# Optimization experiments

Measured on AMD Instinct MI355X. Metric: run time of the kernel, lower is better.

## Reference

```python
import jax, jax.numpy as jnp
import numpy as np

TOPK = 2
ROUTE_SCALE = 1.0


def setup_inputs() -> dict:
    key = jax.random.key(0)
    ks = jax.random.split(key, 9)
    B, T, C, E, H = 4, 2048, 1024, 8, 2752
    s = 0.02  # init scale for weights
    return {
        "x": jax.random.normal(ks[0], (B, T, C), dtype=jnp.float32),
        "gate_w": jax.random.normal(ks[1], (E, C), dtype=jnp.float32) * s,
        "expert_bias": jnp.zeros((E,), dtype=jnp.float32),
        "w1": jax.random.normal(ks[2], (E, C, H), dtype=jnp.float32) * s,
        "w2": jax.random.normal(ks[3], (E, H, C), dtype=jnp.float32) * s,
        "w3": jax.random.normal(ks[4], (E, C, H), dtype=jnp.float32) * s,
        "sw1": jax.random.normal(ks[5], (C, H), dtype=jnp.float32) * s,
        "sw2": jax.random.normal(ks[6], (H, C), dtype=jnp.float32) * s,
        "sw3": jax.random.normal(ks[7], (C, H), dtype=jnp.float32) * s,
    }


def reference(x, gate_w, expert_bias, w1, w2, w3, sw1, sw2, sw3):
    B, T, C = x.shape
    E = gate_w.shape[0]
    xf = x.reshape(-1, C)  # (N, C)
    N = xf.shape[0]

    # --- ExpertGate (sigmoid scoring, aux-loss-free, eval mode) ---
    scores = jax.nn.sigmoid(xf @ gate_w.T)            # (N, E), original scores
    routing = scores + expert_bias[None, :]           # bias only affects selection
    _, idx = jax.lax.top_k(routing, TOPK)             # (N, TOPK)
    w = jnp.take_along_axis(scores, idx, axis=1)      # gather original scores
    w = w / (w.sum(axis=-1, keepdims=True) + 1e-8)    # sigmoid normalization
    w = w * ROUTE_SCALE

    # Scatter top-k weights into a dense (N, E) combine matrix
    gates = jnp.zeros((N, E), dtype=xf.dtype)
    gates = gates.at[jnp.arange(N)[:, None], idx].add(w)

    # --- Routed SwiGLU experts (dense compute, gated combine) ---
    y = jnp.zeros_like(xf)
    for e in range(E):  # small fixed loop over experts
        h = jax.nn.silu(xf @ w1[e]) * (xf @ w3[e])    # (N, H)
        y = y + gates[:, e:e + 1] * (h @ w2[e])

    # --- Shared expert (always on) ---
    y = y + (jax.nn.silu(xf @ sw1) * (xf @ sw3)) @ sw2

    return y.reshape(B, T, C)
```

## Files before the change

### kernel.cpp

```cpp
#include <hip/hip_runtime.h>
#include <hip/hip_bf16.h>
#include <stdint.h>

#define E_ 8
#define C_ 1024
#define H_ 2752
#define NTOK 8192
#define CAP_ROWS 17408

typedef unsigned short u16;
typedef __attribute__((ext_vector_type(8))) short bf16x8;
typedef __attribute__((ext_vector_type(4))) float f32x4;

static constexpr size_t SZ_XB    = (size_t)NTOK * C_ * 2;
static constexpr size_t SZ_WT    = (size_t)E_ * H_ * C_ * 2;
static constexpr size_t SZ_SWT   = (size_t)H_ * C_ * 2;
static constexpr size_t SZ_H     = (size_t)CAP_ROWS * H_ * 2;

static constexpr size_t OFF_XB   = 0;
static constexpr size_t OFF_W1T  = OFF_XB   + SZ_XB;
static constexpr size_t OFF_W3T  = OFF_W1T  + SZ_WT;
static constexpr size_t OFF_W2T  = OFF_W3T  + SZ_WT;
static constexpr size_t OFF_SW1T = OFF_W2T  + SZ_WT;
static constexpr size_t OFF_SW3T = OFF_SW1T + SZ_SWT;
static constexpr size_t OFF_SW2T = OFF_SW3T + SZ_SWT;
static constexpr size_t OFF_H    = OFF_SW2T + SZ_SWT;
static constexpr size_t OFF_RIDX = OFF_H    + SZ_H;
static constexpr size_t OFF_RW   = OFF_RIDX + (size_t)NTOK*2*4;
static constexpr size_t OFF_OFFS = OFF_RW   + (size_t)NTOK*2*4;
static constexpr size_t OFF_PTOK = OFF_OFFS + 64;
static constexpr size_t OFF_PW   = OFF_PTOK + (size_t)CAP_ROWS*4;
static constexpr size_t WS_NEED  = OFF_PW   + (size_t)CAP_ROWS*4;

__device__ __forceinline__ u16 f2bf(float f) {
  union { float f; uint32_t u; } v; v.f = f;
  uint32_t r = v.u + 0x7FFFu + ((v.u >> 16) & 1u);
  return (u16)(r >> 16);
}

__device__ __forceinline__ void gld16(const void* g, const void* l) {
  uint32_t lo = (uint32_t)(uintptr_t)l;
  lo = __builtin_amdgcn_readfirstlane(lo);
  __builtin_amdgcn_global_load_lds(
      (const __attribute__((address_space(1))) void*)g,
      (__attribute__((address_space(3))) void*)(uintptr_t)lo, 16, 0, 0);
}

#define MFMA16(A,B,C) __builtin_amdgcn_mfma_f32_16x16x32_bf16((A),(B),(C),0,0,0)

__global__ __launch_bounds__(256) void gate_kernel(
    const float* __restrict__ x, const float* __restrict__ gw,
    const float* __restrict__ bias, u16* __restrict__ xb,
    int* __restrict__ ridx, float* __restrict__ rw)
{
  const int n = blockIdx.x, t = threadIdx.x;
  const float4 v = *(const float4*)(x + (size_t)n * C_ + t * 4);
  union { u16 u[4]; uint2 d; } pk;
  pk.u[0] = f2bf(v.x); pk.u[1] = f2bf(v.y); pk.u[2] = f2bf(v.z); pk.u[3] = f2bf(v.w);
  *(uint2*)(xb + (size_t)n * C_ + t * 4) = pk.d;

  float p[E_];
#pragma unroll
  for (int e = 0; e < E_; ++e) {
    const float4 g = *(const float4*)(gw + (size_t)e * C_ + t * 4);
    p[e] = v.x * g.x + v.y * g.y + v.z * g.z + v.w * g.w;
  }
#pragma unroll
  for (int e = 0; e < E_; ++e)
    for (int off = 32; off > 0; off >>= 1) p[e] += __shfl_down(p[e], off);

  __shared__ float red[4][E_];
  const int wv = t >> 6;
  if ((t & 63) == 0) {
#pragma unroll
    for (int e = 0; e < E_; ++e) red[wv][e] = p[e];
  }
  __syncthreads();
  if (t == 0) {
    float sc[E_], rt[E_];
#pragma unroll
    for (int e = 0; e < E_; ++e) {
      const float d = red[0][e] + red[1][e] + red[2][e] + red[3][e];
      const float s = 1.f / (1.f + expf(-d));
      sc[e] = s; rt[e] = s + bias[e];
    }
    int i0 = 0; float b0 = rt[0];
#pragma unroll
    for (int e = 1; e < E_; ++e) if (rt[e] > b0) { b0 = rt[e]; i0 = e; }
    int i1 = -1; float b1 = -1e30f;
#pragma unroll
    for (int e = 0; e < E_; ++e) if (e != i0 && rt[e] > b1) { b1 = rt[e]; i1 = e; }
    const float s0 = sc[i0], s1 = sc[i1];
    const float inv = 1.f / (s0 + s1 + 1e-8f);
    ridx[2 * n] = i0; ridx[2 * n + 1] = i1;
    rw[2 * n] = s0 * inv; rw[2 * n + 1] = s1 * inv;
  }
}

__global__ __launch_bounds__(256) void transpose_cs_kernel(
    const float* __restrict__ w1, const float* __restrict__ w3,
    const float* __restrict__ sw1, const float* __restrict__ sw3,
    u16* __restrict__ w1t, u16* __restrict__ w3t,
    u16* __restrict__ sw1t, u16* __restrict__ sw3t)
{
  const int z = blockIdx.z;
  const float* src; u16* dst;
  if      (z < 8)  { src = w1 + (size_t)z * C_ * H_;       dst = w1t + (size_t)z * H_ * C_; }
  else if (z < 16) { src = w3 + (size_t)(z - 8) * C_ * H_; dst = w3t + (size_t)(z - 8) * H_ * C_; }
  else if (z == 16){ src = sw1; dst = sw1t; }
  else             { src = sw3; dst = sw3t; }
  __shared__ float tile[32][33];
  const int tx = threadIdx.x, ty = threadIdx.y;
  const int s0 = blockIdx.x * 32;
  const int r0 = blockIdx.y * 32;
#pragma unroll
  for (int i = 0; i < 4; ++i)
    tile[ty + 8 * i][tx] = src[(size_t)(r0 + ty + 8 * i) * H_ + s0 + tx];
  __syncthreads();
#pragma unroll
  for (int i = 0; i < 4; ++i)
    dst[(size_t)(s0 + ty + 8 * i) * C_ + r0 + tx] = f2bf(tile[tx][ty + 8 * i]);
}

__global__ __launch_bounds__(256) void transpose_sc_kernel(
    const float* __restrict__ w2, const float* __restrict__ sw2,
    u16* __restrict__ w2t, u16* __restrict__ sw2t)
{
  const int z = blockIdx.z;
  const float* src; u16* dst;
  if (z < 8) { src = w2 + (size_t)z * H_ * C_; dst = w2t + (size_t)z * C_ * H_; }
  else       { src = sw2; dst = sw2t; }
  __shared__ float tile[32][33];
  const int tx = threadIdx.x, ty = threadIdx.y;
  const int s0 = blockIdx.x * 32;
  const int r0 = blockIdx.y * 32;
#pragma unroll
  for (int i = 0; i < 4; ++i)
    tile[ty + 8 * i][tx] = src[(size_t)(r0 + ty + 8 * i) * C_ + s0 + tx];
  __syncthreads();
#pragma unroll
  for (int i = 0; i < 4; ++i)
    dst[(size_t)(s0 + ty + 8 * i) * H_ + r0 + tx] = f2bf(tile[tx][ty + 8 * i]);
}

__global__ __launch_bounds__(256) void route_scan_kernel(
    const int* __restrict__ ridx, const float* __restrict__ rw,
    int* __restrict__ offsets, int* __restrict__ perm_tok, float* __restrict__ perm_w)
{
  __shared__ int cnt[256][E_];
  __shared__ int pref[E_][257];
  __shared__ int offs[E_ + 1];
  __shared__ int totals[E_];
  const int t = threadIdx.x;
#pragma unroll
  for (int e = 0; e < E_; ++e) cnt[t][e] = 0;
  for (int j = 0; j < 64; ++j) { const int e = ridx[t * 64 + j]; cnt[t][e]++; }
  __syncthreads();
  if (t < E_) {
    int run = 0;
    for (int i = 0; i < 256; ++i) { pref[t][i] = run; run += cnt[i][t]; }
    totals[t] = run; pref[t][256] = run;
  }
  __syncthreads();
  if (t == 0) {
    int o = 0;
    for (int e = 0; e < E_; ++e) { offs[e] = o; o += (totals[e] + 127) & ~127; }
    offs[E_] = o;
    for (int i = 0; i <= E_; ++i) offsets[i] = offs[i];
  }
  __syncthreads();
#pragma unroll
  for (int e = 0; e < E_; ++e) cnt[t][e] = offs[e] + pref[e][t];
  for (int j = 0; j < 64; ++j) {
    const int a = t * 64 + j;
    const int e = ridx[a];
    const int p = cnt[t][e]++;
    perm_tok[p] = a >> 1;
    perm_w[p] = rw[a];
  }
  __syncthreads();
  for (int e = 0; e < E_; ++e) {
    for (int p = offs[e] + totals[e] + t; p < offs[e + 1]; p += 256) {
      perm_tok[p] = 0; perm_w[p] = 0.f;
    }
  }
}

template<int GATHER>
__global__ __launch_bounds__(256, 2) void gemm1_kernel(
    const u16* __restrict__ xb, const u16* __restrict__ w1t_all,
    const u16* __restrict__ w3t_all, u16* __restrict__ hout,
    const int* __restrict__ offsets, const int* __restrict__ perm_tok)
{
  __shared__ u16 lds[3 * 8192];
  const int t = threadIdx.x;
  const int row0 = blockIdx.x * 128;
  const int n0 = blockIdx.y * 128;
  int e = 0;
  if (GATHER) {
    if (row0 >= offsets[8]) return;
#pragma unroll
    for (int i = 0; i < 7; ++i) if (row0 >= offsets[i + 1]) e = i + 1;
  }
  const u16* w1t = GATHER ? (w1t_all + (size_t)e * (H_ * C_)) : w1t_all;
  const u16* w3t = GATHER ? (w3t_all + (size_t)e * (H_ * C_)) : w3t_all;

  const int tq = t >> 3;
  const int cb = (((t & 7) ^ (tq & 7)) << 4);
  const char* gA[4]; const char* gB1[4]; const char* gB3[4];
#pragma unroll
  for (int i = 0; i < 4; ++i) {
    const int m = i * 32 + tq;
    const int tok = GATHER ? perm_tok[row0 + m] : (row0 + m);
    gA[i]  = (const char*)xb  + (size_t)tok * (C_ * 2) + cb;
    const int nn = n0 + m;
    gB1[i] = (const char*)w1t + (size_t)nn * (C_ * 2) + cb;
    gB3[i] = (const char*)w3t + (size_t)nn * (C_ * 2) + cb;
  }
  char* lwave = (char*)lds + (t >> 6) * 1024;

  f32x4 acc1[4][4], acc3[4][4];
#pragma unroll
  for (int i = 0; i < 4; ++i)
#pragma unroll
    for (int j = 0; j < 4; ++j) { acc1[i][j] = f32x4{0.f,0.f,0.f,0.f}; acc3[i][j] = f32x4{0.f,0.f,0.f,0.f}; }

  const int lane = t & 63;
  const int l15 = lane & 15, lhi = lane >> 4, swz = lane & 7;
  const int wm = (t >> 7) & 1, wn = (t >> 6) & 1;
  int arow[4], brow[4];
#pragma unroll
  for (int f = 0; f < 4; ++f) {
    arow[f] = (wm * 64 + f * 16 + l15) * 128;
    brow[f] = (wn * 64 + f * 16 + l15) * 128;
  }
  const char* ldsc = (const char*)lds;

  for (int kt = 0; kt < C_ / 64; ++kt) {
    const int kb = kt * 128;
#pragma unroll
    for (int i = 0; i < 4; ++i) gld16(gA[i]  + kb, lwave + i * 4096);
#pragma unroll
    for (int i = 0; i < 4; ++i) gld16(gB1[i] + kb, lwave + 16384 + i * 4096);
#pragma unroll
    for (int i = 0; i < 4; ++i) gld16(gB3[i] + kb, lwave + 32768 + i * 4096);
    __syncthreads();
#pragma unroll
    for (int kk = 0; kk < 2; ++kk) {
      const int co = ((((kk << 2) | lhi)) ^ swz) << 4;
      bf16x8 a[4], b1[4], b3[4];
#pragma unroll
      for (int f = 0; f < 4; ++f) a[f]  = *(const bf16x8*)(ldsc + arow[f] + co);
#pragma unroll
      for (int f = 0; f < 4; ++f) b1[f] = *(const bf16x8*)(ldsc + 16384 + brow[f] + co);
#pragma unroll
      for (int f = 0; f < 4; ++f) b3[f] = *(const bf16x8*)(ldsc + 32768 + brow[f] + co);
#pragma unroll
      for (int mf = 0; mf < 4; ++mf)
#pragma unroll
        for (int nf = 0; nf < 4; ++nf) {
          acc1[mf][nf] = MFMA16(a[mf], b1[nf], acc1[mf][nf]);
          acc3[mf][nf] = MFMA16(a[mf], b3[nf], acc3[mf][nf]);
        }
    }
    __syncthreads();
  }

  const int rbase = row0 + wm * 64 + lhi * 4;
  const int cbase = n0 + wn * 64 + l15;
#pragma unroll
  for (int mf = 0; mf < 4; ++mf)
#pragma unroll
    for (int q = 0; q < 4; ++q) {
      const int r = rbase + mf * 16 + q;
      u16* hrow = hout + (size_t)r * H_;
#pragma unroll
      for (int nf = 0; nf < 4; ++nf) {
        const int c = cbase + nf * 16;
        if (c < H_) {
          const float v1 = acc1[mf][nf][q], v3 = acc3[mf][nf][q];
          const float sv = v1 / (1.f + __expf(-v1));
          hrow[c] = f2bf(sv * v3);
        }
      }
    }
}

template<int MODE>
__global__ __launch_bounds__(256, 2) void gemm2_kernel(
    const u16* __restrict__ hin, const u16* __restrict__ w2t_all,
    float* __restrict__ y, const int* __restrict__ offsets,
    const int* __restrict__ perm_tok, const float* __restrict__ perm_w)
{
  __shared__ u16 lds[2 * 8192];
  const int t = threadIdx.x;
  const int row0 = blockIdx.x * 128;
  const int n0 = blockIdx.y * 128;
  int e = 0;
  if (MODE == 1) {
    if (row0 >= offsets[8]) return;
#pragma unroll
    for (int i = 0; i < 7; ++i) if (row0 >= offsets[i + 1]) e = i + 1;
  }
  const u16* w2t = (MODE == 1) ? (w2t_all + (size_t)e * (C_ * H_)) : w2t_all;

  const int tq = t >> 3;
  const int cb = (((t & 7) ^ (tq & 7)) << 4);
  const char* gA[4]; const char* gB[4];
#pragma unroll
  for (int i = 0; i < 4; ++i) {
    gA[i] = (const char*)hin + (size_t)(row0 + i * 32 + tq) * (H_ * 2) + cb;
    gB[i] = (const char*)w2t + (size_t)(n0  + i * 32 + tq) * (H_ * 2) + cb;
  }
  char* lwave = (char*)lds + (t >> 6) * 1024;

  f32x4 acc[4][4];
#pragma unroll
  for (int i = 0; i < 4; ++i)
#pragma unroll
    for (int j = 0; j < 4; ++j) acc[i][j] = f32x4{0.f,0.f,0.f,0.f};

  const int lane = t & 63;
  const int l15 = lane & 15, lhi = lane >> 4, swz = lane & 7;
  const int wm = (t >> 7) & 1, wn = (t >> 6) & 1;
  int arow[4], brow[4];
#pragma unroll
  for (int f = 0; f < 4; ++f) {
    arow[f] = (wm * 64 + f * 16 + l15) * 128;
    brow[f] = (wn * 64 + f * 16 + l15) * 128;
  }
  const char* ldsc = (const char*)lds;

  for (int kt = 0; kt < H_ / 64; ++kt) {
    const int kb = kt * 128;
#pragma unroll
    for (int i = 0; i < 4; ++i) gld16(gA[i] + kb, lwave + i * 4096);
#pragma unroll
    for (int i = 0; i < 4; ++i) gld16(gB[i] + kb, lwave + 16384 + i * 4096);
    __syncthreads();
#pragma unroll
    for (int kk = 0; kk < 2; ++kk) {
      const int co = ((((kk << 2) | lhi)) ^ swz) << 4;
      bf16x8 a[4], b[4];
#pragma unroll
      for (int f = 0; f < 4; ++f) a[f] = *(const bf16x8*)(ldsc + arow[f] + co);
#pragma unroll
      for (int f = 0; f < 4; ++f) b[f] = *(const bf16x8*)(ldsc + 16384 + brow[f] + co);
#pragma unroll
      for (int mf = 0; mf < 4; ++mf)
#pragma unroll
        for (int nf = 0; nf < 4; ++nf)
          acc[mf][nf] = MFMA16(a[mf], b[nf], acc[mf][nf]);
    }
    __syncthreads();
  }

  const int rbase = row0 + wm * 64 + lhi * 4;
  const int cbase = n0 + wn * 64 + l15;
#pragma unroll
  for (int mf = 0; mf < 4; ++mf)
#pragma unroll
    for (int q = 0; q < 4; ++q) {
      const int r = rbase + mf * 16 + q;
      if (MODE == 0) {
        float* yr = y + (size_t)r * C_;
#pragma unroll
        for (int nf = 0; nf < 4; ++nf) yr[cbase + nf * 16] = acc[mf][nf][q];
      } else {
        const float wgt = perm_w[r];
        if (wgt != 0.f) {
          const int tok = perm_tok[r];
          float* yr = y + (size_t)tok * C_;
#pragma unroll
          for (int nf = 0; nf < 4; ++nf)
            atomicAdd(yr + cbase + nf * 16, wgt * acc[mf][nf][q]);
        }
      }
    }
}

extern "C" void kernel_launch(void* const* d_in, const int* in_sizes, int n_in,
                              void* d_out, int out_size, void* d_ws, size_t ws_size,
                              hipStream_t stream)
{
  const float* x    = (const float*)d_in[0];
  const float* gw   = (const float*)d_in[1];
  const float* bias = (const float*)d_in[2];
  const float* w1   = (const float*)d_in[3];
  const float* w2   = (const float*)d_in[4];
  const float* w3   = (const float*)d_in[5];
  const float* sw1  = (const float*)d_in[6];
  const float* sw2  = (const float*)d_in[7];
  const float* sw3  = (const float*)d_in[8];
  float* y = (float*)d_out;
  char* ws = (char*)d_ws;
  if (ws_size < WS_NEED) return;

  u16*   xb    = (u16*)(ws + OFF_XB);
  u16*   w1t   = (u16*)(ws + OFF_W1T);
  u16*   w3t   = (u16*)(ws + OFF_W3T);
  u16*   w2t   = (u16*)(ws + OFF_W2T);
  u16*   sw1t  = (u16*)(ws + OFF_SW1T);
  u16*   sw3t  = (u16*)(ws + OFF_SW3T);
  u16*   sw2t  = (u16*)(ws + OFF_SW2T);
  u16*   hbuf  = (u16*)(ws + OFF_H);
  int*   ridx  = (int*)(ws + OFF_RIDX);
  float* rwt   = (float*)(ws + OFF_RW);
  int*   offs  = (int*)(ws + OFF_OFFS);
  int*   ptok  = (int*)(ws + OFF_PTOK);
  float* pw    = (float*)(ws + OFF_PW);

  gate_kernel<<<NTOK, 256, 0, stream>>>(x, gw, bias, xb, ridx, rwt);
  transpose_cs_kernel<<<dim3(H_ / 32, C_ / 32, 18), dim3(32, 8), 0, stream>>>(
      w1, w3, sw1, sw3, w1t, w3t, sw1t, sw3t);
  transpose_sc_kernel<<<dim3(C_ / 32, H_ / 32, 9), dim3(32, 8), 0, stream>>>(
      w2, sw2, w2t, sw2t);
  route_scan_kernel<<<1, 256, 0, stream>>>(ridx, rwt, offs, ptok, pw);

  gemm1_kernel<0><<<dim3(NTOK / 128, 22), 256, 0, stream>>>(
      xb, sw1t, sw3t, hbuf, nullptr, nullptr);
  gemm2_kernel<0><<<dim3(NTOK / 128, 8), 256, 0, stream>>>(
      hbuf, sw2t, y, nullptr, nullptr, nullptr);
  gemm1_kernel<1><<<dim3(CAP_ROWS / 128, 22), 256, 0, stream>>>(
      xb, w1t, w3t, hbuf, offs, ptok);
  gemm2_kernel<1><<<dim3(CAP_ROWS / 128, 8), 256, 0, stream>>>(
      hbuf, w2t, y, offs, ptok, pw);
}
```

Baseline: 671.9 us.

## Rewrite expert GEMMs as 256x128 tiles with 8-wave pipelined LDS prefetch

Replaces the 128x128 tile GEMMs with 512-thread, 256x128-tile kernels that double-buffer K-slices in LDS. Global-to-LDS loads are issued ahead of the MFMA work using explicit vmcnt waits, raw barriers and setprio. The shared-expert and routed-expert first GEMMs are merged into a single launch, and routing capacity is padded to 256-row blocks. The K tail of the second GEMM reads from a zeroed pad buffer instead of branching. This aims to hide memory latency and raise MFMA utilisation, at the cost of more padded rows, a much larger LDS footprint, and fragile hand-tuned synchronisation.

Result: slower. 786.8 us (+17.1%).

```diff
diff --git a/kernel.cpp b/kernel.cpp
--- a/kernel.cpp
+++ b/kernel.cpp
@@ -6,7 +6,11 @@
 #define C_ 1024
 #define H_ 2752
 #define NTOK 8192
-#define CAP_ROWS 17408
+#define CAP_ROWS 18432
+#define ROUTED_MB 72
+#define SHARED_MB 32
+#define SHARED_HBASE 18432
+#define HROWS 26624
 
 typedef unsigned short u16;
 typedef __attribute__((ext_vector_type(8))) short bf16x8;
@@ -15,7 +19,7 @@
 static constexpr size_t SZ_XB    = (size_t)NTOK * C_ * 2;
 static constexpr size_t SZ_WT    = (size_t)E_ * H_ * C_ * 2;
 static constexpr size_t SZ_SWT   = (size_t)H_ * C_ * 2;
-static constexpr size_t SZ_H     = (size_t)CAP_ROWS * H_ * 2;
+static constexpr size_t SZ_H     = (size_t)HROWS * H_ * 2;
 
 static constexpr size_t OFF_XB   = 0;
 static constexpr size_t OFF_W1T  = OFF_XB   + SZ_XB;
@@ -25,7 +29,8 @@
 static constexpr size_t OFF_SW3T = OFF_SW1T + SZ_SWT;
 static constexpr size_t OFF_SW2T = OFF_SW3T + SZ_SWT;
 static constexpr size_t OFF_H    = OFF_SW2T + SZ_SWT;
-static constexpr size_t OFF_RIDX = OFF_H    + SZ_H;
+static constexpr size_t OFF_ZP   = OFF_H    + SZ_H;
+static constexpr size_t OFF_RIDX = OFF_ZP   + 16384;
 static constexpr size_t OFF_RW   = OFF_RIDX + (size_t)NTOK*2*4;
 static constexpr size_t OFF_OFFS = OFF_RW   + (size_t)NTOK*2*4;
 static constexpr size_t OFF_PTOK = OFF_OFFS + 64;
@@ -38,7 +43,7 @@
   return (u16)(r >> 16);
 }
 
-__device__ __forceinline__ void gld16(const void* g, const void* l) {
+__device__ __forceinline__ void gld16(const void* g, void* l) {
   uint32_t lo = (uint32_t)(uintptr_t)l;
   lo = __builtin_amdgcn_readfirstlane(lo);
   __builtin_amdgcn_global_load_lds(
@@ -47,6 +52,9 @@
 }
 
 #define MFMA16(A,B,C) __builtin_amdgcn_mfma_f32_16x16x32_bf16((A),(B),(C),0,0,0)
+#define BARX() do { asm volatile("" ::: "memory"); __builtin_amdgcn_s_barrier(); \
+                    asm volatile("" ::: "memory"); } while (0)
+#define VMC(N) asm volatile("s_waitcnt vmcnt(" #N ")" ::: "memory")
 
 __global__ __launch_bounds__(256) void gate_kernel(
     const float* __restrict__ x, const float* __restrict__ gw,
@@ -164,7 +172,7 @@
   __syncthreads();
   if (t == 0) {
     int o = 0;
-    for (int e = 0; e < E_; ++e) { offs[e] = o; o += (totals[e] + 127) & ~127; }
+    for (int e = 0; e < E_; ++e) { offs[e] = o; o += (totals[e] + 255) & ~255; }
     offs[E_] = o;
     for (int i = 0; i <= E_; ++i) offsets[i] = offs[i];
   }
@@ -186,197 +194,251 @@
   }
 }
 
-template<int GATHER>
-__global__ __launch_bounds__(256, 2) void gemm1_kernel(
+__global__ __launch_bounds__(512, 2) void gemm1_8p(
     const u16* __restrict__ xb, const u16* __restrict__ w1t_all,
-    const u16* __restrict__ w3t_all, u16* __restrict__ hout,
-    const int* __restrict__ offsets, const int* __restrict__ perm_tok)
-{
-  __shared__ u16 lds[3 * 8192];
+    const u16* __restrict__ w3t_all, const u16* __restrict__ sw1t,
+    const u16* __restrict__ sw3t, u16* __restrict__ hbuf,
+    const int* __restrict__ offsets, const int* __restrict__ ptok)
+{
+  __shared__ char lds[131072];
   const int t = threadIdx.x;
-  const int row0 = blockIdx.x * 128;
+  const int bx = blockIdx.x;
   const int n0 = blockIdx.y * 128;
-  int e = 0;
-  if (GATHER) {
+
+  const u16 *b1w, *b3w; int row0; size_t hr0; int gather;
+  if (bx < ROUTED_MB) {
+    row0 = bx * 256;
     if (row0 >= offsets[8]) return;
+    int e = 0;
 #pragma unroll
     for (int i = 0; i < 7; ++i) if (row0 >= offsets[i + 1]) e = i + 1;
-  }
-  const u16* w1t = GATHER ? (w1t_all + (size_t)e * (H_ * C_)) : w1t_all;
-  const u16* w3t = GATHER ? (w3t_all + (size_t)e * (H_ * C_)) : w3t_all;
-
-  const int tq = t >> 3;
-  const int cb = (((t & 7) ^ (tq & 7)) << 4);
-  const char* gA[4]; const char* gB1[4]; const char* gB3[4];
-#pragma unroll
-  for (int i = 0; i < 4; ++i) {
-    const int m = i * 32 + tq;
-    const int tok = GATHER ? perm_tok[row0 + m] : (row0 + m);
-    gA[i]  = (const char*)xb  + (size_t)tok * (C_ * 2) + cb;
-    const int nn = n0 + m;
-    gB1[i] = (const char*)w1t + (size_t)nn * (C_ * 2) + cb;
-    gB3[i] = (const char*)w3t + (size_t)nn * (C_ * 2) + cb;
-  }
-  char* lwave = (char*)lds + (t >> 6) * 1024;
-
-  f32x4 acc1[4][4], acc3[4][4];
-#pragma unroll
-  for (int i = 0; i < 4; ++i)
-#pragma unroll
-    for (int j = 0; j < 4; ++j) { acc1[i][j] = f32x4{0.f,0.f,0.f,0.f}; acc3[i][j] = f32x4{0.f,0.f,0.f,0.f}; }
-
-  const int lane = t & 63;
-  const int l15 = lane & 15, lhi = lane >> 4, swz = lane & 7;
-  const int wm = (t >> 7) & 1, wn = (t >> 6) & 1;
-  int arow[4], brow[4];
-#pragma unroll
-  for (int f = 0; f < 4; ++f) {
-    arow[f] = (wm * 64 + f * 16 + l15) * 128;
-    brow[f] = (wn * 64 + f * 16 + l15) * 128;
-  }
-  const char* ldsc = (const char*)lds;
-
-  for (int kt = 0; kt < C_ / 64; ++kt) {
-    const int kb = kt * 128;
-#pragma unroll
-    for (int i = 0; i < 4; ++i) gld16(gA[i]  + kb, lwave + i * 4096);
-#pragma unroll
-    for (int i = 0; i < 4; ++i) gld16(gB1[i] + kb, lwave + 16384 + i * 4096);
-#pragma unroll
-    for (int i = 0; i < 4; ++i) gld16(gB3[i] + kb, lwave + 32768 + i * 4096);
-    __syncthreads();
-#pragma unroll
-    for (int kk = 0; kk < 2; ++kk) {
-      const int co = ((((kk << 2) | lhi)) ^ swz) << 4;
-      bf16x8 a[4], b1[4], b3[4];
-#pragma unroll
-      for (int f = 0; f < 4; ++f) a[f]  = *(const bf16x8*)(ldsc + arow[f] + co);
-#pragma unroll
-      for (int f = 0; f < 4; ++f) b1[f] = *(const bf16x8*)(ldsc + 16384 + brow[f] + co);
-#pragma unroll
-      for (int f = 0; f < 4; ++f) b3[f] = *(const bf16x8*)(ldsc + 32768 + brow[f] + co);
-#pragma unroll
-      for (int mf = 0; mf < 4; ++mf)
-#pragma unroll
-        for (int nf = 0; nf < 4; ++nf) {
-          acc1[mf][nf] = MFMA16(a[mf], b1[nf], acc1[mf][nf]);
-          acc3[mf][nf] = MFMA16(a[mf], b3[nf], acc3[mf][nf]);
-        }
-    }
-    __syncthreads();
-  }
-
-  const int rbase = row0 + wm * 64 + lhi * 4;
-  const int cbase = n0 + wn * 64 + l15;
-#pragma unroll
-  for (int mf = 0; mf < 4; ++mf)
+    b1w = w1t_all + (size_t)e * (H_ * C_);
+    b3w = w3t_all + (size_t)e * (H_ * C_);
+    hr0 = (size_t)row0; gather = 1;
+  } else {
+    row0 = (bx - ROUTED_MB) * 256;
+    b1w = sw1t; b3w = sw3t; hr0 = (size_t)SHARED_HBASE + row0; gather = 0;
+  }
+
+  const int sr = t >> 2, sc = (t & 3) << 4;
+  const int ta0 = gather ? ptok[row0 + sr]       : (row0 + sr);
+  const int ta1 = gather ? ptok[row0 + 128 + sr] : (row0 + 128 + sr);
+  const char* aS0 = (const char*)xb + (size_t)ta0 * 2048 + sc;
+  const char* aS1 = (const char*)xb + (size_t)ta1 * 2048 + sc;
+  int nb = n0 + sr; if (nb > H_ - 1) nb = H_ - 1;
+  const char* b1S = (const char*)b1w + (size_t)nb * 2048 + sc;
+  const char* b3S = (const char*)b3w + (size_t)nb * 2048 + sc;
+  const int wb = (t >> 6) << 10;
+  char* ldsp = (char*)lds;
+
+#define ARG(kt,kh)  ((((kt)&1)*2+(kh))*16384)
+#define B1RG(kt,kh) (65536 + ((((kt)&1)*2+(kh))*8192))
+#define B3RG(kt,kh) (98304 + ((((kt)&1)*2+(kh))*8192))
+#define SA(kt,kh) do { const int go=(kt)*128+(kh)*64; \
+  gld16(aS0+go, ldsp+ARG(kt,kh)+wb); gld16(aS1+go, ldsp+ARG(kt,kh)+8192+wb); } while(0)
+#define SB(kt,kh) do { const int go=(kt)*128+(kh)*64; \
+  gld16(b1S+go, ldsp+B1RG(kt,kh)+wb); gld16(b3S+go, ldsp+B3RG(kt,kh)+wb); } while(0)
+
+  const int lane = t & 63, l15 = lane & 15, lhi = lane >> 4;
+  const int wv = t >> 6, wm = wv >> 2, wn = wv & 3;
+  int aoff[8], boff[2];
+#pragma unroll
+  for (int mf = 0; mf < 8; ++mf) aoff[mf] = (wm * 128 + mf * 16 + l15) * 64 + lhi * 16;
+#pragma unroll
+  for (int nf = 0; nf < 2; ++nf) boff[nf] = (wn * 32 + nf * 16 + l15) * 64 + lhi * 16;
+
+  bf16x8 a[4], rb1[2], rb3[2];
+  f32x4 acc1[8][2], acc3[8][2];
+#pragma unroll
+  for (int i = 0; i < 8; ++i)
+#pragma unroll
+    for (int j = 0; j < 2; ++j) { acc1[i][j] = f32x4{0,0,0,0}; acc3[i][j] = f32x4{0,0,0,0}; }
+
+#define LB(kt,kh) do { \
+  rb1[0]=*(const bf16x8*)(ldsp+B1RG(kt,kh)+boff[0]); \
+  rb1[1]=*(const bf16x8*)(ldsp+B1RG(kt,kh)+boff[1]); \
+  rb3[0]=*(const bf16x8*)(ldsp+B3RG(kt,kh)+boff[0]); \
+  rb3[1]=*(const bf16x8*)(ldsp+B3RG(kt,kh)+boff[1]); } while(0)
+#define LA(kt,kh,mh) do { \
+  a[0]=*(const bf16x8*)(ldsp+ARG(kt,kh)+aoff[(mh)*4+0]); \
+  a[1]=*(const bf16x8*)(ldsp+ARG(kt,kh)+aoff[(mh)*4+1]); \
+  a[2]=*(const bf16x8*)(ldsp+ARG(kt,kh)+aoff[(mh)*4+2]); \
+  a[3]=*(const bf16x8*)(ldsp+ARG(kt,kh)+aoff[(mh)*4+3]); } while(0)
+#define MM(mh) do { __builtin_amdgcn_s_setprio(1); \
+  _Pragma("unroll") for (int mf = 0; mf < 4; ++mf) \
+    _Pragma("unroll") for (int nf = 0; nf < 2; ++nf) { \
+      acc1[(mh)*4+mf][nf] = MFMA16(a[mf], rb1[nf], acc1[(mh)*4+mf][nf]); \
+      acc3[(mh)*4+mf][nf] = MFMA16(a[mf], rb3[nf], acc3[(mh)*4+mf][nf]); } \
+  __builtin_amdgcn_s_setprio(0); } while(0)
+
+  SA(0,0); SA(0,1); SB(0,0); SB(0,1); SA(1,0); SB(1,0);
+  VMC(4); BARX();
+
+#pragma unroll 1
+  for (int i = 0; i < 8; ++i) {
+    const int k0 = 2*i, k1 = k0+1, k2 = k0+2, k3 = k0+3;
+    const bool more = (i < 7);
+    LB(k0,0); LA(k0,0,0); SA(k1,1); SB(k1,1);
+    BARX(); MM(0); BARX();
+    LA(k0,0,1);
+    BARX(); MM(1); BARX();
+    LB(k0,1); LA(k0,1,0); if (more) SA(k2,0);
+    BARX(); MM(0); BARX();
+    LA(k0,1,1); if (more) SB(k2,0);
+    BARX(); MM(1); VMC(4); BARX();
+    LB(k1,0); LA(k1,0,0); if (more) { SA(k2,1); SB(k2,1); }
+    BARX(); MM(0); BARX();
+    LA(k1,0,1);
+    BARX(); MM(1); BARX();
+    LB(k1,1); LA(k1,1,0); if (more) SA(k3,0);
+    BARX(); MM(0); BARX();
+    LA(k1,1,1); if (more) SB(k3,0);
+    BARX(); MM(1); VMC(4); BARX();
+  }
+
+  const int rb_ = wm * 128 + lhi * 4;
+  const int cb_ = n0 + wn * 32 + l15;
+#pragma unroll
+  for (int mf = 0; mf < 8; ++mf)
 #pragma unroll
     for (int q = 0; q < 4; ++q) {
-      const int r = rbase + mf * 16 + q;
-      u16* hrow = hout + (size_t)r * H_;
-#pragma unroll
-      for (int nf = 0; nf < 4; ++nf) {
-        const int c = cbase + nf * 16;
+      const int r = rb_ + mf * 16 + q;
+      u16* hrow = hbuf + (hr0 + r) * H_;
+#pragma unroll
+      for (int nf = 0; nf < 2; ++nf) {
+        const int c = cb_ + nf * 16;
         if (c < H_) {
           const float v1 = acc1[mf][nf][q], v3 = acc3[mf][nf][q];
-          const float sv = v1 / (1.f + __expf(-v1));
-          hrow[c] = f2bf(sv * v3);
+          hrow[c] = f2bf((v1 / (1.f + __expf(-v1))) * v3);
         }
       }
     }
+#undef ARG
+#undef B1RG
+#undef B3RG
+#undef SA
+#undef SB
+#undef LB
+#undef LA
+#undef MM
 }
 
 template<int MODE>
-__global__ __launch_bounds__(256, 2) void gemm2_kernel(
-    const u16* __restrict__ hin, const u16* __restrict__ w2t_all,
+__global__ __launch_bounds__(512, 2) void gemm2_8p(
+    const u16* __restrict__ hbuf, const u16* __restrict__ w2t_all,
     float* __restrict__ y, const int* __restrict__ offsets,
-    const int* __restrict__ perm_tok, const float* __restrict__ perm_w)
-{
-  __shared__ u16 lds[2 * 8192];
+    const int* __restrict__ ptok, const float* __restrict__ pw,
+    const char* __restrict__ zp)
+{
+  __shared__ char lds[98304];
   const int t = threadIdx.x;
-  const int row0 = blockIdx.x * 128;
+  const int bx = blockIdx.x;
   const int n0 = blockIdx.y * 128;
-  int e = 0;
+
+  int row0 = bx * 256; size_t hr0; const u16* bW;
   if (MODE == 1) {
     if (row0 >= offsets[8]) return;
+    int e = 0;
 #pragma unroll
     for (int i = 0; i < 7; ++i) if (row0 >= offsets[i + 1]) e = i + 1;
-  }
-  const u16* w2t = (MODE == 1) ? (w2t_all + (size_t)e * (C_ * H_)) : w2t_all;
-
-  const int tq = t >> 3;
-  const int cb = (((t & 7) ^ (tq & 7)) << 4);
-  const char* gA[4]; const char* gB[4];
-#pragma unroll
-  for (int i = 0; i < 4; ++i) {
-    gA[i] = (const char*)hin + (size_t)(row0 + i * 32 + tq) * (H_ * 2) + cb;
-    gB[i] = (const char*)w2t + (size_t)(n0  + i * 32 + tq) * (H_ * 2) + cb;
-  }
-  char* lwave = (char*)lds + (t >> 6) * 1024;
-
-  f32x4 acc[4][4];
-#pragma unroll
-  for (int i = 0; i < 4; ++i)
-#pragma unroll
-    for (int j = 0; j < 4; ++j) acc[i][j] = f32x4{0.f,0.f,0.f,0.f};
-
-  const int lane = t & 63;
-  const int l15 = lane & 15, lhi = lane >> 4, swz = lane & 7;
-  const int wm = (t >> 7) & 1, wn = (t >> 6) & 1;
-  int arow[4], brow[4];
-#pragma unroll
-  for (int f = 0; f < 4; ++f) {
-    arow[f] = (wm * 64 + f * 16 + l15) * 128;
-    brow[f] = (wn * 64 + f * 16 + l15) * 128;
-  }
-  const char* ldsc = (const char*)lds;
-
-  for (int kt = 0; kt < H_ / 64; ++kt) {
-    const int kb = kt * 128;
-#pragma unroll
-    for (int i = 0; i < 4; ++i) gld16(gA[i] + kb, lwave + i * 4096);
-#pragma unroll
-    for (int i = 0; i < 4; ++i) gld16(gB[i] + kb, lwave + 16384 + i * 4096);
-    __syncthreads();
-#pragma unroll
-    for (int kk = 0; kk < 2; ++kk) {
-      const int co = ((((kk << 2) | lhi)) ^ swz) << 4;
-      bf16x8 a[4], b[4];
-#pragma unroll
-      for (int f = 0; f < 4; ++f) a[f] = *(const bf16x8*)(ldsc + arow[f] + co);
-#pragma unroll
-      for (int f = 0; f < 4; ++f) b[f] = *(const bf16x8*)(ldsc + 16384 + brow[f] + co);
-#pragma unroll
-      for (int mf = 0; mf < 4; ++mf)
-#pragma unroll
-        for (int nf = 0; nf < 4; ++nf)
-          acc[mf][nf] = MFMA16(a[mf], b[nf], acc[mf][nf]);
-    }
-    __syncthreads();
-  }
-
-  const int rbase = row0 + wm * 64 + lhi * 4;
-  const int cbase = n0 + wn * 64 + l15;
-#pragma unroll
-  for (int mf = 0; mf < 4; ++mf)
+    bW = w2t_all + (size_t)e * (C_ * H_);
+    hr0 = (size_t)row0;
+  } else {
+    bW = w2t_all;
+    hr0 = (size_t)SHARED_HBASE + row0;
+  }
+
+  const int sr = t >> 2, sc = (t & 3) << 4;
+  const char* aS0 = (const char*)hbuf + (hr0 + sr) * (size_t)(H_ * 2) + sc;
+  const char* aS1 = (const char*)hbuf + (hr0 + 128 + sr) * (size_t)(H_ * 2) + sc;
+  const char* bS  = (const char*)bW + (size_t)(n0 + sr) * (H_ * 2) + sc;
+  const int wb = (t >> 6) << 10;
+  char* ldsp = (char*)lds;
+  const char* zpa = zp + t * 16;
+  const char* zpb = zp + t * 16;
+
+#define A2RG(kt,kh) ((((kt)&1)*2+(kh))*16384)
+#define B2RG(kt,kh) (65536 + ((((kt)&1)*2+(kh))*8192))
+#define SA2(kt,kh) do { if ((kt) < 43) { const int go=(kt)*128+(kh)*64; \
+    gld16(aS0+go, ldsp+A2RG(kt,kh)+wb); gld16(aS1+go, ldsp+A2RG(kt,kh)+8192+wb); } \
+  else { gld16(zpa, ldsp+A2RG(kt,kh)+wb); gld16(zpa, ldsp+A2RG(kt,kh)+8192+wb); } } while(0)
+#define SB2(kt,kh) do { if ((kt) < 43) { const int go=(kt)*128+(kh)*64; \
+    gld16(bS+go, ldsp+B2RG(kt,kh)+wb); } \
+  else { gld16(zpb, ldsp+B2RG(kt,kh)+wb); } } while(0)
+
+  const int lane = t & 63, l15 = lane & 15, lhi = lane >> 4;
+  const int wv = t >> 6, wm = wv >> 2, wn = wv & 3;
+  int aoff[8], boff[2];
+#pragma unroll
+  for (int mf = 0; mf < 8; ++mf) aoff[mf] = (wm * 128 + mf * 16 + l15) * 64 + lhi * 16;
+#pragma unroll
+  for (int nf = 0; nf < 2; ++nf) boff[nf] = (wn * 32 + nf * 16 + l15) * 64 + lhi * 16;
+
+  bf16x8 a8[8], rb[2];
+  f32x4 acc[8][2];
+#pragma unroll
+  for (int i = 0; i < 8; ++i)
+#pragma unroll
+    for (int j = 0; j < 2; ++j) acc[i][j] = f32x4{0,0,0,0};
+
+#define LB2(kt,kh) do { \
+  rb[0]=*(const bf16x8*)(ldsp+B2RG(kt,kh)+boff[0]); \
+  rb[1]=*(const bf16x8*)(ldsp+B2RG(kt,kh)+boff[1]); } while(0)
+#define LA8(kt,kh) do { \
+  _Pragma("unroll") for (int mf = 0; mf < 8; ++mf) \
+    a8[mf]=*(const bf16x8*)(ldsp+A2RG(kt,kh)+aoff[mf]); } while(0)
+#define MM2() do { __builtin_amdgcn_s_setprio(1); \
+  _Pragma("unroll") for (int mf = 0; mf < 8; ++mf) \
+    _Pragma("unroll") for (int nf = 0; nf < 2; ++nf) \
+      acc[mf][nf] = MFMA16(a8[mf], rb[nf], acc[mf][nf]); \
+  __builtin_amdgcn_s_setprio(0); } while(0)
+
+  SA2(0,0); SA2(0,1); SB2(0,0); SB2(0,1); SA2(1,0); SB2(1,0);
+  VMC(3); BARX();
+
+#pragma unroll 1
+  for (int i = 0; i < 22; ++i) {
+    const int k0 = 2*i, k1 = k0+1, k2 = k0+2, k3 = k0+3;
+    const bool more = (i < 21);
+    LB2(k0,0); LA8(k0,0); SA2(k1,1); SB2(k1,1);
+    BARX(); MM2(); BARX();
+    LB2(k0,1); LA8(k0,1); if (more) { SA2(k2,0); SB2(k2,0); }
+    BARX(); MM2(); VMC(3); BARX();
+    LB2(k1,0); LA8(k1,0); if (more) { SA2(k2,1); SB2(k2,1); }
+    BARX(); MM2(); BARX();
+    LB2(k1,1); LA8(k1,1); if (more) { SA2(k3,0); SB2(k3,0); }
+    BARX(); MM2(); VMC(3); BARX();
+  }
+
+  const int rb_ = wm * 128 + lhi * 4;
+  const int cb_ = n0 + wn * 32 + l15;
+#pragma unroll
+  for (int mf = 0; mf < 8; ++mf)
 #pragma unroll
     for (int q = 0; q < 4; ++q) {
-      const int r = rbase + mf * 16 + q;
+      const int r = rb_ + mf * 16 + q;
       if (MODE == 0) {
-        float* yr = y + (size_t)r * C_;
-#pragma unroll
-        for (int nf = 0; nf < 4; ++nf) yr[cbase + nf * 16] = acc[mf][nf][q];
+        float* yr = y + (size_t)(row0 + r) * C_;
+#pragma unroll
+        for (int nf = 0; nf < 2; ++nf) yr[cb_ + nf * 16] = acc[mf][nf][q];
       } else {
-        const float wgt = perm_w[r];
+        const float wgt = pw[row0 + r];
         if (wgt != 0.f) {
-          const int tok = perm_tok[r];
+          const int tok = ptok[row0 + r];
           float* yr = y + (size_t)tok * C_;
 #pragma unroll
-          for (int nf = 0; nf < 4; ++nf)
-            atomicAdd(yr + cbase + nf * 16, wgt * acc[mf][nf][q]);
+          for (int nf = 0; nf < 2; ++nf)
+            atomicAdd(yr + cb_ + nf * 16, wgt * acc[mf][nf][q]);
         }
       }
     }
+#undef A2RG
+#undef B2RG
+#undef SA2
+#undef SB2
+#undef LB2
+#undef LA8
+#undef MM2
 }
 
 extern "C" void kernel_launch(void* const* d_in, const int* in_sizes, int n_in,
@@ -404,12 +466,14 @@
   u16*   sw3t  = (u16*)(ws + OFF_SW3T);
   u16*   sw2t  = (u16*)(ws + OFF_SW2T);
   u16*   hbuf  = (u16*)(ws + OFF_H);
+  char*  zp    = ws + OFF_ZP;
   int*   ridx  = (int*)(ws + OFF_RIDX);
   float* rwt   = (float*)(ws + OFF_RW);
   int*   offs  = (int*)(ws + OFF_OFFS);
   int*   ptok  = (int*)(ws + OFF_PTOK);
   float* pw    = (float*)(ws + OFF_PW);
 
+  hipMemsetAsync(zp, 0, 16384, stream);
   gate_kernel<<<NTOK, 256, 0, stream>>>(x, gw, bias, xb, ridx, rwt);
   transpose_cs_kernel<<<dim3(H_ / 32, C_ / 32, 18), dim3(32, 8), 0, stream>>>(
       w1, w3, sw1, sw3, w1t, w3t, sw1t, sw3t);
@@ -417,12 +481,10 @@
       w2, sw2, w2t, sw2t);
   route_scan_kernel<<<1, 256, 0, stream>>>(ridx, rwt, offs, ptok, pw);
 
-  gemm1_kernel<0><<<dim3(NTOK / 128, 22), 256, 0, stream>>>(
-      xb, sw1t, sw3t, hbuf, nullptr, nullptr);
-  gemm2_kernel<0><<<dim3(NTOK / 128, 8), 256, 0, stream>>>(
-      hbuf, sw2t, y, nullptr, nullptr, nullptr);
-  gemm1_kernel<1><<<dim3(CAP_ROWS / 128, 22), 256, 0, stream>>>(
-      xb, w1t, w3t, hbuf, offs, ptok);
-  gemm2_kernel<1><<<dim3(CAP_ROWS / 128, 8), 256, 0, stream>>>(
-      hbuf, w2t, y, offs, ptok, pw);
-}
+  gemm1_8p<<<dim3(ROUTED_MB + SHARED_MB, 22), 512, 0, stream>>>(
+      xb, w1t, w3t, sw1t, sw3t, hbuf, offs, ptok);
+  gemm2_8p<0><<<dim3(SHARED_MB, 8), 512, 0, stream>>>(
+      hbuf, sw2t, y, offs, ptok, pw, zp);
+  gemm2_8p<1><<<dim3(ROUTED_MB, 8), 512, 0, stream>>>(
+      hbuf, w2t, y, offs, ptok, pw, zp);
+}
```

## Switch GEMMs to 32x32 MFMA and merge shared and routed experts into single launches

Applied to the files above, without the earlier changes.

Both GEMM kernels move from 16x16x32 to 32x32x16 bf16 MFMA tiles, with fewer, larger accumulator fragments per wave. The shared-expert and routed-expert GEMMs are fused into one launch each by extending the grid, so shared rows use a separate region of the enlarged H buffer. The shared output is now accumulated with atomics, which requires a memset of y first. The aim is higher MFMA throughput per LDS read and fewer launches and tail effects, at the cost of extra atomics for the shared path and a larger workspace.

New measurement: 732.2 us. 9.0% more time.

```diff
diff --git a/kernel.cpp b/kernel.cpp
--- a/kernel.cpp
+++ b/kernel.cpp
@@ -7,15 +7,19 @@
 #define H_ 2752
 #define NTOK 8192
 #define CAP_ROWS 17408
+#define ROUTED_XB1 136
+#define SHARED_XB1 64
+#define SHARED_HBASE 17408
+#define HROWS 25600
 
 typedef unsigned short u16;
 typedef __attribute__((ext_vector_type(8))) short bf16x8;
-typedef __attribute__((ext_vector_type(4))) float f32x4;
+typedef __attribute__((ext_vector_type(16))) float f32x16;
 
 static constexpr size_t SZ_XB    = (size_t)NTOK * C_ * 2;
 static constexpr size_t SZ_WT    = (size_t)E_ * H_ * C_ * 2;
 static constexpr size_t SZ_SWT   = (size_t)H_ * C_ * 2;
-static constexpr size_t SZ_H     = (size_t)CAP_ROWS * H_ * 2;
+static constexpr size_t SZ_H     = (size_t)HROWS * H_ * 2;
 
 static constexpr size_t OFF_XB   = 0;
 static constexpr size_t OFF_W1T  = OFF_XB   + SZ_XB;
@@ -38,7 +42,7 @@
   return (u16)(r >> 16);
 }
 
-__device__ __forceinline__ void gld16(const void* g, const void* l) {
+__device__ __forceinline__ void gld16(const void* g, void* l) {
   uint32_t lo = (uint32_t)(uintptr_t)l;
   lo = __builtin_amdgcn_readfirstlane(lo);
   __builtin_amdgcn_global_load_lds(
@@ -46,7 +50,7 @@
       (__attribute__((address_space(3))) void*)(uintptr_t)lo, 16, 0, 0);
 }
 
-#define MFMA16(A,B,C) __builtin_amdgcn_mfma_f32_16x16x32_bf16((A),(B),(C),0,0,0)
+#define MFMA32(A,B,C) __builtin_amdgcn_mfma_f32_32x32x16_bf16((A),(B),(C),0,0,0)
 
 __global__ __launch_bounds__(256) void gate_kernel(
     const float* __restrict__ x, const float* __restrict__ gw,
@@ -186,24 +190,31 @@
   }
 }
 
-template<int GATHER>
-__global__ __launch_bounds__(256, 2) void gemm1_kernel(
+__global__ __launch_bounds__(256, 2) void gemm1_32(
     const u16* __restrict__ xb, const u16* __restrict__ w1t_all,
-    const u16* __restrict__ w3t_all, u16* __restrict__ hout,
-    const int* __restrict__ offsets, const int* __restrict__ perm_tok)
-{
-  __shared__ u16 lds[3 * 8192];
+    const u16* __restrict__ w3t_all, const u16* __restrict__ sw1t,
+    const u16* __restrict__ sw3t, u16* __restrict__ hbuf,
+    const int* __restrict__ offsets, const int* __restrict__ ptok)
+{
+  __shared__ char lds[49152];
   const int t = threadIdx.x;
-  const int row0 = blockIdx.x * 128;
+  const int bx = blockIdx.x;
   const int n0 = blockIdx.y * 128;
-  int e = 0;
-  if (GATHER) {
+
+  const u16 *b1w, *b3w; int row0; size_t hr0; int gather;
+  if (bx < ROUTED_XB1) {
+    row0 = bx * 128;
     if (row0 >= offsets[8]) return;
+    int e = 0;
 #pragma unroll
     for (int i = 0; i < 7; ++i) if (row0 >= offsets[i + 1]) e = i + 1;
-  }
-  const u16* w1t = GATHER ? (w1t_all + (size_t)e * (H_ * C_)) : w1t_all;
-  const u16* w3t = GATHER ? (w3t_all + (size_t)e * (H_ * C_)) : w3t_all;
+    b1w = w1t_all + (size_t)e * (H_ * C_);
+    b3w = w3t_all + (size_t)e * (H_ * C_);
+    hr0 = (size_t)row0; gather = 1;
+  } else {
+    row0 = (bx - ROUTED_XB1) * 128;
+    b1w = sw1t; b3w = sw3t; hr0 = (size_t)SHARED_HBASE + row0; gather = 0;
+  }
 
   const int tq = t >> 3;
   const int cb = (((t & 7) ^ (tq & 7)) << 4);
@@ -211,170 +222,171 @@
 #pragma unroll
   for (int i = 0; i < 4; ++i) {
     const int m = i * 32 + tq;
-    const int tok = GATHER ? perm_tok[row0 + m] : (row0 + m);
-    gA[i]  = (const char*)xb  + (size_t)tok * (C_ * 2) + cb;
-    const int nn = n0 + m;
-    gB1[i] = (const char*)w1t + (size_t)nn * (C_ * 2) + cb;
-    gB3[i] = (const char*)w3t + (size_t)nn * (C_ * 2) + cb;
-  }
-  char* lwave = (char*)lds + (t >> 6) * 1024;
-
-  f32x4 acc1[4][4], acc3[4][4];
-#pragma unroll
-  for (int i = 0; i < 4; ++i)
-#pragma unroll
-    for (int j = 0; j < 4; ++j) { acc1[i][j] = f32x4{0.f,0.f,0.f,0.f}; acc3[i][j] = f32x4{0.f,0.f,0.f,0.f}; }
-
-  const int lane = t & 63;
-  const int l15 = lane & 15, lhi = lane >> 4, swz = lane & 7;
+    const int tok = gather ? ptok[row0 + m] : (row0 + m);
+    gA[i] = (const char*)xb + (size_t)tok * 2048 + cb;
+    int nn = n0 + m; if (nn > H_ - 1) nn = H_ - 1;
+    gB1[i] = (const char*)b1w + (size_t)nn * 2048 + cb;
+    gB3[i] = (const char*)b3w + (size_t)nn * 2048 + cb;
+  }
+  const int wvb = (t >> 6) << 10;
+  char* ldsp = (char*)lds;
+
+  const int lane = t & 63, l31 = lane & 31, hi = lane >> 5, x7 = lane & 7;
   const int wm = (t >> 7) & 1, wn = (t >> 6) & 1;
-  int arow[4], brow[4];
-#pragma unroll
-  for (int f = 0; f < 4; ++f) {
-    arow[f] = (wm * 64 + f * 16 + l15) * 128;
-    brow[f] = (wn * 64 + f * 16 + l15) * 128;
-  }
-  const char* ldsc = (const char*)lds;
-
-  for (int kt = 0; kt < C_ / 64; ++kt) {
+  int arow[2], brow[2];
+#pragma unroll
+  for (int f = 0; f < 2; ++f) {
+    arow[f] = (wm * 64 + f * 32 + l31) * 128;
+    brow[f] = (wn * 64 + f * 32 + l31) * 128;
+  }
+
+  f32x16 acc1[2][2], acc3[2][2];
+#pragma unroll
+  for (int i = 0; i < 2; ++i)
+#pragma unroll
+    for (int j = 0; j < 2; ++j) {
+      acc1[i][j] = (f32x16)(0.f);
+      acc3[i][j] = (f32x16)(0.f);
+    }
+
+  for (int kt = 0; kt < 16; ++kt) {
     const int kb = kt * 128;
 #pragma unroll
-    for (int i = 0; i < 4; ++i) gld16(gA[i]  + kb, lwave + i * 4096);
-#pragma unroll
-    for (int i = 0; i < 4; ++i) gld16(gB1[i] + kb, lwave + 16384 + i * 4096);
-#pragma unroll
-    for (int i = 0; i < 4; ++i) gld16(gB3[i] + kb, lwave + 32768 + i * 4096);
+    for (int i = 0; i < 4; ++i) gld16(gA[i]  + kb, ldsp + i * 4096 + wvb);
+#pragma unroll
+    for (int i = 0; i < 4; ++i) gld16(gB1[i] + kb, ldsp + 16384 + i * 4096 + wvb);
+#pragma unroll
+    for (int i = 0; i < 4; ++i) gld16(gB3[i] + kb, ldsp + 32768 + i * 4096 + wvb);
     __syncthreads();
 #pragma unroll
-    for (int kk = 0; kk < 2; ++kk) {
-      const int co = ((((kk << 2) | lhi)) ^ swz) << 4;
-      bf16x8 a[4], b1[4], b3[4];
-#pragma unroll
-      for (int f = 0; f < 4; ++f) a[f]  = *(const bf16x8*)(ldsc + arow[f] + co);
-#pragma unroll
-      for (int f = 0; f < 4; ++f) b1[f] = *(const bf16x8*)(ldsc + 16384 + brow[f] + co);
-#pragma unroll
-      for (int f = 0; f < 4; ++f) b3[f] = *(const bf16x8*)(ldsc + 32768 + brow[f] + co);
-#pragma unroll
-      for (int mf = 0; mf < 4; ++mf)
-#pragma unroll
-        for (int nf = 0; nf < 4; ++nf) {
-          acc1[mf][nf] = MFMA16(a[mf], b1[nf], acc1[mf][nf]);
-          acc3[mf][nf] = MFMA16(a[mf], b3[nf], acc3[mf][nf]);
+    for (int kk = 0; kk < 4; ++kk) {
+      const int co = (((2 * kk + hi) ^ x7) << 4);
+      bf16x8 av[2], b1v[2], b3v[2];
+#pragma unroll
+      for (int f = 0; f < 2; ++f) av[f]  = *(const bf16x8*)(ldsp + arow[f] + co);
+#pragma unroll
+      for (int f = 0; f < 2; ++f) b1v[f] = *(const bf16x8*)(ldsp + 16384 + brow[f] + co);
+#pragma unroll
+      for (int f = 0; f < 2; ++f) b3v[f] = *(const bf16x8*)(ldsp + 32768 + brow[f] + co);
+#pragma unroll
+      for (int mf = 0; mf < 2; ++mf)
+#pragma unroll
+        for (int nf = 0; nf < 2; ++nf) {
+          acc1[mf][nf] = MFMA32(av[mf], b1v[nf], acc1[mf][nf]);
+          acc3[mf][nf] = MFMA32(av[mf], b3v[nf], acc3[mf][nf]);
         }
     }
     __syncthreads();
   }
 
-  const int rbase = row0 + wm * 64 + lhi * 4;
-  const int cbase = n0 + wn * 64 + l15;
-#pragma unroll
-  for (int mf = 0; mf < 4; ++mf)
-#pragma unroll
-    for (int q = 0; q < 4; ++q) {
-      const int r = rbase + mf * 16 + q;
-      u16* hrow = hout + (size_t)r * H_;
-#pragma unroll
-      for (int nf = 0; nf < 4; ++nf) {
-        const int c = cbase + nf * 16;
+  const int cbase = n0 + wn * 64 + l31;
+#pragma unroll
+  for (int mf = 0; mf < 2; ++mf)
+#pragma unroll
+    for (int q = 0; q < 16; ++q) {
+      const int r = wm * 64 + mf * 32 + (q & 3) + 8 * (q >> 2) + 4 * hi;
+      u16* hrow = hbuf + (hr0 + r) * H_;
+#pragma unroll
+      for (int nf = 0; nf < 2; ++nf) {
+        const int c = cbase + nf * 32;
         if (c < H_) {
           const float v1 = acc1[mf][nf][q], v3 = acc3[mf][nf][q];
-          const float sv = v1 / (1.f + __expf(-v1));
-          hrow[c] = f2bf(sv * v3);
+          hrow[c] = f2bf((v1 / (1.f + __expf(-v1))) * v3);
         }
       }
     }
 }
 
-template<int MODE>
-__global__ __launch_bounds__(256, 2) void gemm2_kernel(
-    const u16* __restrict__ hin, const u16* __restrict__ w2t_all,
-    float* __restrict__ y, const int* __restrict__ offsets,
-    const int* __restrict__ perm_tok, const float* __restrict__ perm_w)
-{
-  __shared__ u16 lds[2 * 8192];
+__global__ __launch_bounds__(256, 2) void gemm2_32(
+    const u16* __restrict__ hbuf, const u16* __restrict__ w2t_all,
+    const u16* __restrict__ sw2t, float* __restrict__ y,
+    const int* __restrict__ offsets, const int* __restrict__ ptok,
+    const float* __restrict__ pw)
+{
+  __shared__ char lds[32768];
   const int t = threadIdx.x;
-  const int row0 = blockIdx.x * 128;
+  const int bx = blockIdx.x;
   const int n0 = blockIdx.y * 128;
-  int e = 0;
-  if (MODE == 1) {
+
+  int row0; size_t hr0; const u16* bW; int routed;
+  if (bx < ROUTED_XB1) {
+    row0 = bx * 128;
     if (row0 >= offsets[8]) return;
+    int e = 0;
 #pragma unroll
     for (int i = 0; i < 7; ++i) if (row0 >= offsets[i + 1]) e = i + 1;
-  }
-  const u16* w2t = (MODE == 1) ? (w2t_all + (size_t)e * (C_ * H_)) : w2t_all;
+    bW = w2t_all + (size_t)e * (C_ * H_);
+    hr0 = (size_t)row0; routed = 1;
+  } else {
+    row0 = (bx - ROUTED_XB1) * 128;
+    bW = sw2t; hr0 = (size_t)SHARED_HBASE + row0; routed = 0;
+  }
 
   const int tq = t >> 3;
   const int cb = (((t & 7) ^ (tq & 7)) << 4);
   const char* gA[4]; const char* gB[4];
 #pragma unroll
   for (int i = 0; i < 4; ++i) {
-    gA[i] = (const char*)hin + (size_t)(row0 + i * 32 + tq) * (H_ * 2) + cb;
-    gB[i] = (const char*)w2t + (size_t)(n0  + i * 32 + tq) * (H_ * 2) + cb;
-  }
-  char* lwave = (char*)lds + (t >> 6) * 1024;
-
-  f32x4 acc[4][4];
-#pragma unroll
-  for (int i = 0; i < 4; ++i)
-#pragma unroll
-    for (int j = 0; j < 4; ++j) acc[i][j] = f32x4{0.f,0.f,0.f,0.f};
-
-  const int lane = t & 63;
-  const int l15 = lane & 15, lhi = lane >> 4, swz = lane & 7;
+    const int m = i * 32 + tq;
+    gA[i] = (const char*)hbuf + (hr0 + m) * (size_t)(H_ * 2) + cb;
+    gB[i] = (const char*)bW + (size_t)(n0 + m) * (H_ * 2) + cb;
+  }
+  const int wvb = (t >> 6) << 10;
+  char* ldsp = (char*)lds;
+
+  const int lane = t & 63, l31 = lane & 31, hi = lane >> 5, x7 = lane & 7;
   const int wm = (t >> 7) & 1, wn = (t >> 6) & 1;
-  int arow[4], brow[4];
-#pragma unroll
-  for (int f = 0; f < 4; ++f) {
-    arow[f] = (wm * 64 + f * 16 + l15) * 128;
-    brow[f] = (wn * 64 + f * 16 + l15) * 128;
-  }
-  const char* ldsc = (const char*)lds;
-
-  for (int kt = 0; kt < H_ / 64; ++kt) {
+  int arow[2], brow[2];
+#pragma unroll
+  for (int f = 0; f < 2; ++f) {
+    arow[f] = (wm * 64 + f * 32 + l31) * 128;
+    brow[f] = (wn * 64 + f * 32 + l31) * 128;
+  }
+
+  f32x16 acc[2][2];
+#pragma unroll
+  for (int i = 0; i < 2; ++i)
+#pragma unroll
+    for (int j = 0; j < 2; ++j) acc[i][j] = (f32x16)(0.f);
+
+  for (int kt = 0; kt < 43; ++kt) {
     const int kb = kt * 128;
 #pragma unroll
-    for (int i = 0; i < 4; ++i) gld16(gA[i] + kb, lwave + i * 4096);
-#pragma unroll
-    for (int i = 0; i < 4; ++i) gld16(gB[i] + kb, lwave + 16384 + i * 4096);
+    for (int i = 0; i < 4; ++i) gld16(gA[i] + kb, ldsp + i * 4096 + wvb);
+#pragma unroll
+    for (int i = 0; i < 4; ++i) gld16(gB[i] + kb, ldsp + 16384 + i * 4096 + wvb);
     __syncthreads();
 #pragma unroll
-    for (int kk = 0; kk < 2; ++kk) {
-      const int co = ((((kk << 2) | lhi)) ^ swz) << 4;
-      bf16x8 a[4], b[4];
-#pragma unroll
-      for (int f = 0; f < 4; ++f) a[f] = *(const bf16x8*)(ldsc + arow[f] + co);
-#pragma unroll
-      for (int f = 0; f < 4; ++f) b[f] = *(const bf16x8*)(ldsc + 16384 + brow[f] + co);
-#pragma unroll
-      for (int mf = 0; mf < 4; ++mf)
-#pragma unroll
-        for (int nf = 0; nf < 4; ++nf)
-          acc[mf][nf] = MFMA16(a[mf], b[nf], acc[mf][nf]);
+    for (int kk = 0; kk < 4; ++kk) {
+      const int co = (((2 * kk + hi) ^ x7) << 4);
+      bf16x8 av[2], bv[2];
+#pragma unroll
+      for (int f = 0; f < 2; ++f) av[f] = *(const bf16x8*)(ldsp + arow[f] + co);
+#pragma unroll
+      for (int f = 0; f < 2; ++f) bv[f] = *(const bf16x8*)(ldsp + 16384 + brow[f] + co);
+#pragma unroll
+      for (int mf = 0; mf < 2; ++mf)
+#pragma unroll
+        for (int nf = 0; nf < 2; ++nf)
+          acc[mf][nf] = MFMA32(av[mf], bv[nf], acc[mf][nf]);
     }
     __syncthreads();
   }
 
-  const int rbase = row0 + wm * 64 + lhi * 4;
-  const int cbase = n0 + wn * 64 + l15;
-#pragma unroll
-  for (int mf = 0; mf < 4; ++mf)
-#pragma unroll
-    for (int q = 0; q < 4; ++q) {
-      const int r = rbase + mf * 16 + q;
-      if (MODE == 0) {
-        float* yr = y + (size_t)r * C_;
-#pragma unroll
-        for (int nf = 0; nf < 4; ++nf) yr[cbase + nf * 16] = acc[mf][nf][q];
-      } else {
-        const float wgt = perm_w[r];
-        if (wgt != 0.f) {
-          const int tok = perm_tok[r];
-          float* yr = y + (size_t)tok * C_;
-#pragma unroll
-          for (int nf = 0; nf < 4; ++nf)
-            atomicAdd(yr + cbase + nf * 16, wgt * acc[mf][nf][q]);
-        }
+  const int cbase = n0 + wn * 64 + l31;
+#pragma unroll
+  for (int mf = 0; mf < 2; ++mf)
+#pragma unroll
+    for (int q = 0; q < 16; ++q) {
+      const int r = wm * 64 + mf * 32 + (q & 3) + 8 * (q >> 2) + 4 * hi;
+      const int hr = (int)hr0 + r;
+      const float wgt = routed ? pw[hr] : 1.0f;
+      if (wgt != 0.f) {
+        const int tok = routed ? ptok[hr] : (hr - SHARED_HBASE);
+        float* yr = y + (size_t)tok * C_;
+#pragma unroll
+        for (int nf = 0; nf < 2; ++nf)
+          atomicAdd(yr + cbase + nf * 32, wgt * acc[mf][nf][q]);
       }
     }
 }
@@ -410,6 +422,7 @@
   int*   ptok  = (int*)(ws + OFF_PTOK);
   float* pw    = (float*)(ws + OFF_PW);
 
+  hipMemsetAsync(y, 0, (size_t)out_size * 4, stream);
   gate_kernel<<<NTOK, 256, 0, stream>>>(x, gw, bias, xb, ridx, rwt);
   transpose_cs_kernel<<<dim3(H_ / 32, C_ / 32, 18), dim3(32, 8), 0, stream>>>(
       w1, w3, sw1, sw3, w1t, w3t, sw1t, sw3t);
@@ -417,12 +430,8 @@
       w2, sw2, w2t, sw2t);
   route_scan_kernel<<<1, 256, 0, stream>>>(ridx, rwt, offs, ptok, pw);
 
-  gemm1_kernel<0><<<dim3(NTOK / 128, 22), 256, 0, stream>>>(
-      xb, sw1t, sw3t, hbuf, nullptr, nullptr);
-  gemm2_kernel<0><<<dim3(NTOK / 128, 8), 256, 0, stream>>>(
-      hbuf, sw2t, y, nullptr, nullptr, nullptr);
-  gemm1_kernel<1><<<dim3(CAP_ROWS / 128, 22), 256, 0, stream>>>(
-      xb, w1t, w3t, hbuf, offs, ptok);
-  gemm2_kernel<1><<<dim3(CAP_ROWS / 128, 8), 256, 0, stream>>>(
-      hbuf, w2t, y, offs, ptok, pw);
-}
+  gemm1_32<<<dim3(ROUTED_XB1 + SHARED_XB1, 22), 256, 0, stream>>>(
+      xb, w1t, w3t, sw1t, sw3t, hbuf, offs, ptok);
+  gemm2_32<<<dim3(ROUTED_XB1 + SHARED_XB1, 8), 256, 0, stream>>>(
+      hbuf, w2t, sw2t, y, offs, ptok, pw);
+}
```
